# Performance work log

Hardware: AMD Instinct MI355X
Metric: run time of the kernel (lower is better)

Reference implementation:

```python
import jax, jax.numpy as jnp
import numpy as np

H, C = 4, 64            # heads, channels per head (graph_hidden_channels)
GHC = H * C             # concat width = 256
FIN = 32                # num_node_features
NHID = 256
NOUT = 256
NEG_SLOPE = 0.2         # PyG GATConv default negative_slope


def gat_conv(x, src, dst, n, W, a_src, a_dst, bias):
    # x: [N, Fin], W: [Fin, H*C], a_src/a_dst: [H, C], bias: [H*C]
    h = (x @ W).reshape(n, H, C)                       # [N,H,C]
    s = (h * a_src).sum(-1)                            # [N,H] src logits
    d = (h * a_dst).sum(-1)                            # [N,H] dst logits
    e = jax.nn.leaky_relu(s[src] + d[dst], NEG_SLOPE)  # [E,H]
    m = jax.ops.segment_max(e, dst, num_segments=n)    # segment softmax (stable)
    ex = jnp.exp(e - m[dst])
    denom = jax.ops.segment_sum(ex, dst, num_segments=n)
    alpha = ex / jnp.maximum(denom[dst], 1e-16)        # [E,H]
    msg = h[src] * alpha[:, :, None]                   # [E,H,C]
    out = jax.ops.segment_sum(msg, dst, num_segments=n)
    return out.reshape(n, GHC) + bias


def setup_inputs() -> dict:
    key = jax.random.key(0)
    ks = jax.random.split(key, 32)
    N, E, G = 50000, 800000, 256
    inp = {
        'x': jax.random.normal(ks[0], (N, FIN), dtype=jnp.float32),
        'edge_index': jax.random.randint(ks[1], (2, E), 0, N, dtype=jnp.int32),
        'batch': jnp.sort(jax.random.randint(ks[2], (N,), 0, G, dtype=jnp.int32)),
        'num_graphs': G,
    }
    def p(k, shape):
        return jax.random.normal(k, shape, dtype=jnp.float32) * 0.05
    # three GATConv layers + head linears
    ins = [FIN, C, C]
    i = 3
    for l, fin in enumerate(ins, start=1):
        inp[f'W{l}'] = p(ks[i], (fin, GHC)); i += 1
        inp[f'a{l}s'] = p(ks[i], (H, C)); i += 1
        inp[f'a{l}d'] = p(ks[i], (H, C)); i += 1
        inp[f'b{l}'] = p(ks[i], (GHC,)); i += 1
        inp[f'hl{l}_w'] = p(ks[i], (GHC, C)); i += 1
        inp[f'hl{l}_b'] = p(ks[i], (C,)); i += 1
    inp['mh1_w'] = p(ks[i], (C, NHID)); i += 1
    inp['mh1_b'] = p(ks[i], (NHID,)); i += 1
    inp['mh2_w'] = p(ks[i], (NHID, NOUT)); i += 1
    inp['mh2_b'] = p(ks[i], (NOUT,))
    return inp


def reference(x, edge_index, batch, num_graphs,
              W1, a1s, a1d, b1, hl1_w, hl1_b,
              W2, a2s, a2d, b2, hl2_w, hl2_b,
              W3, a3s, a3d, b3, hl3_w, hl3_b,
              mh1_w, mh1_b, mh2_w, mh2_b):
    n = x.shape[0]
    loops = jnp.arange(n, dtype=edge_index.dtype)  # PyG add_self_loops=True
    src = jnp.concatenate([edge_index[0], loops])
    dst = jnp.concatenate([edge_index[1], loops])

    h = gat_conv(x, src, dst, n, W1, a1s, a1d, b1)
    h = jax.nn.relu(h @ hl1_w + hl1_b)
    h = gat_conv(h, src, dst, n, W2, a2s, a2d, b2)
    h = jax.nn.relu(h @ hl2_w + hl2_b)
    h = gat_conv(h, src, dst, n, W3, a3s, a3d, b3)
    h = h @ hl3_w + hl3_b                      # no relu before pooling (as in source)

    sums = jax.ops.segment_sum(h, batch, num_segments=num_graphs)
    cnt = jax.ops.segment_sum(jnp.ones((n,), h.dtype), batch, num_segments=num_graphs)
    g = sums / jnp.maximum(cnt, 1.0)[:, None]  # global_mean_pool

    g = jax.nn.relu(g @ mh1_w + mh1_b)
    return g @ mh2_w + mh2_b
```

## Files before the change

kernel.cpp:

```cpp
#include <hip/hip_runtime.h>
#include <hip/hip_bf16.h>
#include <hip/hip_fp16.h>
#include <math.h>

#define HD 4
#define CH 64
#define GHC 256
#define NEG 0.2f
#define CHUNK 4096
#define BCAP 16384

#define WAVE_SYNC() do { __builtin_amdgcn_wave_barrier(); \
                         asm volatile("s_waitcnt lgkmcnt(0)" ::: "memory"); } while (0)

typedef _Float16 f16x8 __attribute__((ext_vector_type(8)));
typedef float f32x4 __attribute__((ext_vector_type(4)));

__device__ __forceinline__ float wsum32(float v){
  #pragma unroll
  for (int o = 16; o > 0; o >>= 1) v += __shfl_xor(v, o);
  return v;
}

__global__ __launch_bounds__(256)
void bin_stage(const int* __restrict__ ei, int E, int N,
               int* __restrict__ bres, unsigned* __restrict__ pairs)
{
  __shared__ unsigned staged[CHUNK];
  __shared__ unsigned short bkt[CHUNK];
  __shared__ int cnts[256], loff[256], gpos[256];
  const int t = threadIdx.x;
  const int tot = E + N;
  const int cbase = blockIdx.x * CHUNK;
  if (cbase >= tot) return;

  cnts[t] = 0;
  __syncthreads();

  unsigned myp[CHUNK / 256];
  int myb[CHUNK / 256], myr[CHUNK / 256];
  #pragma unroll
  for (int j = 0; j < CHUNK / 256; j++){
    int i = cbase + t + j * 256;
    myb[j] = -1;
    if (i < tot){
      int src, dst;
      if (i < E){ src = ei[i]; dst = ei[E + i]; }
      else { src = dst = i - E; }
      myb[j] = dst >> 8;
      myp[j] = (unsigned)src | ((unsigned)dst << 16);
      myr[j] = atomicAdd(&cnts[myb[j]], 1);
    }
  }
  __syncthreads();

  int v = cnts[t];
  loff[t] = v;
  __syncthreads();
  for (int o = 1; o < 256; o <<= 1){
    int tv = (t >= o) ? loff[t - o] : 0;
    __syncthreads();
    loff[t] += tv;
    __syncthreads();
  }
  int excl = loff[t] - v;
  __syncthreads();
  loff[t] = excl;
  __syncthreads();

  #pragma unroll
  for (int j = 0; j < CHUNK / 256; j++){
    if (myb[j] >= 0){
      int slot = loff[myb[j]] + myr[j];
      staged[slot] = myp[j];
      bkt[slot] = (unsigned short)myb[j];
    }
  }
  if (v > 0) gpos[t] = atomicAdd(&bres[t], v);
  __syncthreads();

  int total = min(CHUNK, tot - cbase);
  for (int i = t; i < total; i += 256){
    int b = bkt[i];
    int addr = b * BCAP + gpos[b] + (i - loff[b]);
    pairs[addr] = staged[i];
  }
}

__global__ __launch_bounds__(256)
void build_csr(const unsigned* __restrict__ pairs, const int* __restrict__ bres,
               int N, int Etot, int* __restrict__ offs, unsigned short* __restrict__ csr)
{
  __shared__ int dcnt[256], doff[256], bscan[256];
  const int b = blockIdx.x, t = threadIdx.x;
  int bv = bres[t];
  bscan[t] = bv;
  __syncthreads();
  for (int o = 1; o < 256; o <<= 1){
    int tv = (t >= o) ? bscan[t - o] : 0;
    __syncthreads();
    bscan[t] += tv;
    __syncthreads();
  }
  const int beg = bscan[b] - bres[b];
  const int cnt = bres[b];
  const unsigned* pb = pairs + (size_t)b * BCAP;
  dcnt[t] = 0;
  __syncthreads();
  for (int i = t; i < cnt; i += 256)
    atomicAdd(&dcnt[(pb[i] >> 16) & 255], 1);
  __syncthreads();
  int v = dcnt[t];
  doff[t] = v;
  __syncthreads();
  for (int o = 1; o < 256; o <<= 1){
    int tv = (t >= o) ? doff[t - o] : 0;
    __syncthreads();
    doff[t] += tv;
    __syncthreads();
  }
  int excl = doff[t] - v;
  __syncthreads();
  doff[t] = excl;
  __syncthreads();
  int node = (b << 8) + t;
  if (node < N) offs[node] = beg + doff[t];
  if (b == 0 && t == 0) offs[N] = Etot;
  dcnt[t] = 0;
  __syncthreads();
  for (int i = t; i < cnt; i += 256){
    unsigned pr = pb[i];
    int l = (pr >> 16) & 255;
    int pos = beg + doff[l] + atomicAdd(&dcnt[l], 1);
    csr[pos] = (unsigned short)(pr & 0xFFFF);
  }
}

__global__ __launch_bounds__(256)
void fuse_all(const float* __restrict__ W1, const float* __restrict__ a1s,
              const float* __restrict__ a1d, const float* __restrict__ b1,
              const float* __restrict__ h1w, const float* __restrict__ h1b,
              const float* __restrict__ W2, const float* __restrict__ a2s,
              const float* __restrict__ a2d, const float* __restrict__ b2,
              const float* __restrict__ h2w, const float* __restrict__ h2b,
              const float* __restrict__ W3, const float* __restrict__ a3s,
              const float* __restrict__ a3d, const float* __restrict__ b3,
              const float* __restrict__ h3w, const float* __restrict__ h3b,
              __half* __restrict__ Wpk1, float* __restrict__ Psd1, float* __restrict__ cb1,
              __half* __restrict__ Wpk2, __half* __restrict__ Ppk2, float* __restrict__ cb2,
              float* __restrict__ Wcp3, __half* __restrict__ Ppk3, float* __restrict__ cb3,
              const int* __restrict__ batch, int N, int G, int* __restrict__ bnd)
{
  const int blk = blockIdx.x, t = threadIdx.x;
  if (blk >= 163){
    int g = (blk - 163) * 256 + t;
    if (g > G) return;
    if (g == G){ bnd[G] = N; return; }
    int lo = 0, hi = N;
    while (lo < hi){ int mid = (lo + hi) >> 1; if (batch[mid] < g) lo = mid + 1; else hi = mid; }
    bnd[g] = lo;
    return;
  }
  const float *W, *as, *ad, *bl, *hlw, *hlb;
  float *cb;
  int FIN, b, layer;
  if (blk < 33){
    W = W1; as = a1s; ad = a1d; bl = b1; hlw = h1w; hlb = h1b;
    cb = cb1; FIN = 32; b = blk; layer = 1;
  } else if (blk < 98){
    W = W2; as = a2s; ad = a2d; bl = b2; hlw = h2w; hlb = h2b;
    cb = cb2; FIN = 64; b = blk - 33; layer = 2;
  } else {
    W = W3; as = a3s; ad = a3d; bl = b3; hlw = h3w; hlb = h3b;
    cb = cb3; FIN = 64; b = blk - 98; layer = 3;
  }
  if (b < FIN){
    const int c = t >> 2, h = t & 3;
    const float* wrow = W + b * GHC + h * 64;
    float acc = 0.f;
    #pragma unroll 8
    for (int j = 0; j < 64; j++)
      acc += wrow[j] * hlw[(h * 64 + j) * CH + c];
    const int k = h * FIN + b;
    if (layer == 3){
      Wcp3[k * CH + c] = acc;
    } else {
      int ks = k >> 5, nt = c >> 4;
      int lane = (((k & 31) >> 3) << 4) | (c & 15);
      int idx = ((ks * 4 + nt) * 64 + lane) * 8 + (k & 7);
      __half* Wpk = (layer == 1) ? Wpk1 : Wpk2;
      Wpk[idx] = __float2half(acc);
    }
    if (t < 8){
      const int hh = t & 3;
      const float* a = (t < 4) ? as : ad;
      const float* wr2 = W + b * GHC + hh * 64;
      float p = 0.f;
      #pragma unroll 8
      for (int j = 0; j < 64; j++) p += wr2[j] * a[hh * 64 + j];
      if (layer == 1){
        Psd1[b * 8 + t] = p;
      } else {
        int kk = b;
        int ks = kk >> 5;
        int lane = (((kk & 31) >> 3) << 4) | t;
        int idx = (ks * 64 + lane) * 8 + (kk & 7);
        __half* Ppk = (layer == 2) ? Ppk2 : Ppk3;
        Ppk[idx] = __float2half(p);
      }
    }
  } else if (t < CH){
    float acc = hlb[t];
    for (int j = 0; j < GHC; j++) acc += bl[j] * hlw[j * CH + t];
    cb[t] = acc;
  }
}

__global__ __launch_bounds__(256)
void logits_from_x(const float* __restrict__ x, const float* __restrict__ Psd,
                   float* __restrict__ s_log, float* __restrict__ d_log,
                   __half* __restrict__ xh0, int N)
{
  int idx = blockIdx.x * 256 + threadIdx.x;
  int node = idx >> 3, q = idx & 7;
  if (node >= N) return;
  const float* xr = x + (size_t)node * 32;
  float v = 0.f;
  #pragma unroll 8
  for (int k = 0; k < 32; k++) v += xr[k] * Psd[k * 8 + q];
  if (q < 4){
    s_log[node * 4 + q] = v;
    __half2 h0 = __floats2half2_rn(xr[q*8+0], xr[q*8+1]);
    __half2 h1 = __floats2half2_rn(xr[q*8+2], xr[q*8+3]);
    __half2 h2 = __floats2half2_rn(xr[q*8+4], xr[q*8+5]);
    __half2 h3 = __floats2half2_rn(xr[q*8+6], xr[q*8+7]);
    uint4 u;
    u.x = *reinterpret_cast<const unsigned*>(&h0);
    u.y = *reinterpret_cast<const unsigned*>(&h1);
    u.z = *reinterpret_cast<const unsigned*>(&h2);
    u.w = *reinterpret_cast<const unsigned*>(&h3);
    *reinterpret_cast<uint4*>(xh0 + (size_t)node * 32 + q * 8) = u;
  } else {
    d_log[node * 4 + (q - 4)] = v;
  }
}

template<int F>
__global__ __launch_bounds__(256)
void gat_aggregate_z(const __half* __restrict__ xin, const float* __restrict__ s_log,
                     const float* __restrict__ d_log, const int* __restrict__ off,
                     const unsigned short* __restrict__ csr, __half* __restrict__ z, int N)
{
  __shared__ float4 qa[4][2][32];
  __shared__ int    qs[4][2][32];
  const int wv   = threadIdx.x >> 6;
  const int lane = threadIdx.x & 63;
  const int half = lane >> 5;
  const int l32  = lane & 31;
  const int n = blockIdx.x * 8 + wv * 2 + half;
  const bool valid = n < N;

  int beg = 0, deg = 0;
  if (valid){ beg = off[n]; deg = off[n + 1] - beg; }

  float d4[4] = {0.f, 0.f, 0.f, 0.f};
  if (valid){
    float4 d4v = reinterpret_cast<const float4*>(d_log)[n];
    d4[0] = d4v.x; d4[1] = d4v.y; d4[2] = d4v.z; d4[3] = d4v.w;
  }

  float den[4], ex[4];
  int s = 0;

  {
    const bool act = valid && (l32 < deg);
    if (act){
      s = csr[beg + l32];
      float4 sl = reinterpret_cast<const float4*>(s_log)[s];
      float t[4] = {sl.x, sl.y, sl.z, sl.w};
      #pragma unroll
      for (int i = 0; i < 4; i++){
        float u = t[i] + d4[i]; u = (u >= 0.f) ? u : NEG * u;
        ex[i] = __expf(u);
      }
    } else {
      #pragma unroll
      for (int i = 0; i < 4; i++) ex[i] = 0.f;
    }
    #pragma unroll
    for (int i = 0; i < 4; i++) den[i] = wsum32(ex[i]);
  }
  for (int base = 32; base < deg; base += 32){
    const int k = base + l32;
    float e2[4] = {0.f, 0.f, 0.f, 0.f};
    if (k < deg){
      int s2 = csr[beg + k];
      float4 sl = reinterpret_cast<const float4*>(s_log)[s2];
      float t[4] = {sl.x, sl.y, sl.z, sl.w};
      #pragma unroll
      for (int i = 0; i < 4; i++){
        float u = t[i] + d4[i]; u = (u >= 0.f) ? u : NEG * u;
        e2[i] = __expf(u);
      }
    }
    #pragma unroll
    for (int i = 0; i < 4; i++) den[i] += wsum32(e2[i]);
  }

  float dninv[4];
  #pragma unroll
  for (int i = 0; i < 4; i++) dninv[i] = 1.f / fmaxf(den[i], 1e-16f);

  float a0[4] = {0.f,0.f,0.f,0.f};
  float a1[4] = {0.f,0.f,0.f,0.f};

  const float4* qap = qa[wv][half];
  const int*    qsp = qs[wv][half];

  auto accum = [&](int cnt){
    int cntR = (cnt + 3) & ~3;
    if (F == 64){
      const __half* xb = xin + 2 * l32;
      for (int e0 = 0; e0 < cntR; e0 += 4){
        float4 al[4]; int sv[4]; unsigned uv[4];
        #pragma unroll
        for (int j = 0; j < 4; j++){
          al[j] = qap[e0 + j];
          sv[j] = qsp[e0 + j];
        }
        #pragma unroll
        for (int j = 0; j < 4; j++)
          uv[j] = *reinterpret_cast<const unsigned*>(xb + sv[j] * 64);
        #pragma unroll
        for (int j = 0; j < 4; j++){
          float2 f = __half22float2(*reinterpret_cast<const __half2*>(&uv[j]));
          a0[0] += al[j].x * f.x; a1[0] += al[j].x * f.y;
          a0[1] += al[j].y * f.x; a1[1] += al[j].y * f.y;
          a0[2] += al[j].z * f.x; a1[2] += al[j].z * f.y;
          a0[3] += al[j].w * f.x; a1[3] += al[j].w * f.y;
        }
      }
    } else {
      const __half* xb = xin + l32;
      for (int e0 = 0; e0 < cntR; e0 += 4){
        float4 al[4]; int sv[4]; __half hv[4];
        #pragma unroll
        for (int j = 0; j < 4; j++){
          al[j] = qap[e0 + j];
          sv[j] = qsp[e0 + j];
        }
        #pragma unroll
        for (int j = 0; j < 4; j++)
          hv[j] = xb[sv[j] * 32];
        #pragma unroll
        for (int j = 0; j < 4; j++){
          float xv = __half2float(hv[j]);
          a0[0] += al[j].x * xv;
          a0[1] += al[j].y * xv;
          a0[2] += al[j].z * xv;
          a0[3] += al[j].w * xv;
        }
      }
    }
  };

  if (deg <= 32){
    qa[wv][half][l32] = make_float4(ex[0] * dninv[0], ex[1] * dninv[1],
                                    ex[2] * dninv[2], ex[3] * dninv[3]);
    qs[wv][half][l32] = s;
    WAVE_SYNC();
    accum(deg);
  } else {
    for (int base = 0; base < deg; base += 32){
      const int k = base + l32;
      int s2 = 0; float al[4] = {0.f, 0.f, 0.f, 0.f};
      if (k < deg){
        s2 = csr[beg + k];
        float4 sl = reinterpret_cast<const float4*>(s_log)[s2];
        float t[4] = {sl.x, sl.y, sl.z, sl.w};
        #pragma unroll
        for (int i = 0; i < 4; i++){
          float u = t[i] + d4[i]; u = (u >= 0.f) ? u : NEG * u;
          al[i] = __expf(u) * dninv[i];
        }
      }
      qa[wv][half][l32] = make_float4(al[0], al[1], al[2], al[3]);
      qs[wv][half][l32] = s2;
      WAVE_SYNC();
      accum(min(32, deg - base));
      WAVE_SYNC();
    }
  }

  if (valid){
    if (F == 64){
      const size_t zb = (size_t)n * 256 + 2 * l32;
      #pragma unroll
      for (int h = 0; h < 4; h++){
        __half2 hv = __floats2half2_rn(a0[h], a1[h]);
        *reinterpret_cast<unsigned*>(z + zb + h * 64) =
            *reinterpret_cast<const unsigned*>(&hv);
      }
    } else {
      const size_t zb = (size_t)n * 128 + l32;
      #pragma unroll
      for (int h = 0; h < 4; h++)
        z[zb + h * 32] = __float2half(a0[h]);
    }
  }
}

template<int ZW>
__global__ __launch_bounds__(256)
void z_transform_mfma(const __half* __restrict__ z, const __half* __restrict__ Wpk,
                      const float* __restrict__ cb, const __half* __restrict__ Ppk,
                      __half* __restrict__ xo, float* __restrict__ s_log,
                      float* __restrict__ d_log, int N)
{
  __shared__ float outs[4][16][68];
  __shared__ float cbs[64];
  const int tid = threadIdx.x;
  const int wv = tid >> 6, lane = tid & 63;
  const int row = lane & 15, kg = lane >> 4;
  const int n0 = blockIdx.x * 64 + wv * 16;
  if (tid < 64) cbs[tid] = cb[tid];
  __syncthreads();

  f32x4 acc0 = {0.f,0.f,0.f,0.f}, acc1 = {0.f,0.f,0.f,0.f};
  f32x4 acc2 = {0.f,0.f,0.f,0.f}, acc3 = {0.f,0.f,0.f,0.f};
  const __half* za = z + (size_t)(n0 + row) * ZW + kg * 8;
  const f16x8* wp = reinterpret_cast<const f16x8*>(Wpk) + lane;
  #pragma unroll
  for (int ks = 0; ks < ZW / 32; ks++){
    f16x8 af = *reinterpret_cast<const f16x8*>(za + ks * 32);
    acc0 = __builtin_amdgcn_mfma_f32_16x16x32_f16(af, wp[(ks*4+0)*64], acc0, 0,0,0);
    acc1 = __builtin_amdgcn_mfma_f32_16x16x32_f16(af, wp[(ks*4+1)*64], acc1, 0,0,0);
    acc2 = __builtin_amdgcn_mfma_f32_16x16x32_f16(af, wp[(ks*4+2)*64], acc2, 0,0,0);
    acc3 = __builtin_amdgcn_mfma_f32_16x16x32_f16(af, wp[(ks*4+3)*64], acc3, 0,0,0);
  }
  #pragma unroll
  for (int r = 0; r < 4; r++){
    int rr = kg * 4 + r;
    outs[wv][rr][ 0 + row] = fmaxf(acc0[r] + cbs[ 0 + row], 0.f);
    outs[wv][rr][16 + row] = fmaxf(acc1[r] + cbs[16 + row], 0.f);
    outs[wv][rr][32 + row] = fmaxf(acc2[r] + cbs[32 + row], 0.f);
    outs[wv][rr][48 + row] = fmaxf(acc3[r] + cbs[48 + row], 0.f);
  }
  WAVE_SYNC();

  #pragma unroll
  for (int i = 0; i < 4; i++){
    int idx = lane + 64 * i;
    int nn = idx >> 4, part = idx & 15;
    int node = n0 + nn;
    if (node < N){
      const float* o = &outs[wv][nn][part * 4];
      __half2 h0 = __floats2half2_rn(o[0], o[1]);
      __half2 h1 = __floats2half2_rn(o[2], o[3]);
      uint2 u;
      u.x = *reinterpret_cast<const unsigned*>(&h0);
      u.y = *reinterpret_cast<const unsigned*>(&h1);
      *reinterpret_cast<uint2*>(xo + (size_t)node * 64 + part * 4) = u;
    }
  }

  f32x4 lacc = {0.f,0.f,0.f,0.f};
  const f16x8* pp = reinterpret_cast<const f16x8*>(Ppk) + lane;
  #pragma unroll
  for (int ks = 0; ks < 2; ks++){
    f16x8 af;
    #pragma unroll
    for (int j = 0; j < 8; j++) af[j] = (_Float16)outs[wv][row][ks * 32 + kg * 8 + j];
    lacc = __builtin_amdgcn_mfma_f32_16x16x32_f16(af, pp[ks * 64], lacc, 0,0,0);
  }
  if (row < 8){
    float* dst = (row < 4) ? s_log : d_log;
    int q = row & 3;
    #pragma unroll
    for (int r = 0; r < 4; r++){
      int node = n0 + kg * 4 + r;
      if (node < N) dst[node * 4 + q] = lacc[r];
    }
  }
}

__global__ __launch_bounds__(256)
void pool_partial(const __half* __restrict__ z3, const int* __restrict__ bnd,
                  float* __restrict__ psum)
{
  const int blk = blockIdx.x, tid = threadIdx.x;
  const int g = blk >> 2, part = blk & 3;
  const int s = bnd[g], e = bnd[g + 1];
  const int cp = tid & 127, rp = tid >> 7;
  float ax = 0.f, ay = 0.f;
  for (int n = s + part + 4 * rp; n < e; n += 8){
    __half2 hv = *reinterpret_cast<const __half2*>(z3 + (size_t)n * 256 + 2 * cp);
    float2 f = __half22float2(hv);
    ax += f.x; ay += f.y;
  }
  __shared__ float shx[2][128], shy[2][128];
  shx[rp][cp] = ax; shy[rp][cp] = ay;
  __syncthreads();
  if (tid < 128){
    psum[(size_t)blk * 256 + 2 * tid]     = shx[0][tid] + shx[1][tid];
    psum[(size_t)blk * 256 + 2 * tid + 1] = shy[0][tid] + shy[1][tid];
  }
}

__global__ __launch_bounds__(256)
void head_mlp(const float* __restrict__ psum, const int* __restrict__ bnd,
              const float* __restrict__ Wcp3, const float* __restrict__ cb3,
              const float* __restrict__ m1w, const float* __restrict__ m1b,
              const float* __restrict__ m2w, const float* __restrict__ m2b,
              float* __restrict__ out)
{
  const int g = blockIdx.x, tid = threadIdx.x;
  const float cnt = (float)max(bnd[g + 1] - bnd[g], 1);
  __shared__ float zbar[256];
  const float* pb = psum + (size_t)g * 1024;
  zbar[tid] = (pb[tid] + pb[256 + tid] + pb[512 + tid] + pb[768 + tid]) / cnt;
  __syncthreads();
  const int c = tid & 63, part = tid >> 6;
  float tp = 0.f;
  #pragma unroll 8
  for (int k = part * 64; k < part * 64 + 64; k++) tp += zbar[k] * Wcp3[k * 64 + c];
  __shared__ float tsh[4][64];
  tsh[part][c] = tp;
  __syncthreads();
  __shared__ float tvec[64];
  if (tid < 64)
    tvec[tid] = tsh[0][tid] + tsh[1][tid] + tsh[2][tid] + tsh[3][tid] + cb3[tid];
  __syncthreads();
  float a = m1b[tid];
  #pragma unroll 8
  for (int cc = 0; cc < 64; cc++) a += tvec[cc] * m1w[cc * 256 + tid];
  __shared__ float g1row[256];
  g1row[tid] = fmaxf(a, 0.f);
  __syncthreads();
  float o = m2b[tid];
  #pragma unroll 8
  for (int k = 0; k < 256; k++) o += g1row[k] * m2w[k * 256 + tid];
  out[g * 256 + tid] = o;
}

extern "C" void kernel_launch(void* const* d_in, const int* in_sizes, int n_in,
                              void* d_out, int out_size, void* d_ws, size_t ws_size,
                              hipStream_t stream)
{
  const float* x     = (const float*)d_in[0];
  const int*   ei    = (const int*)d_in[1];
  const int*   batch = (const int*)d_in[2];
  const float* W1  = (const float*)d_in[4];
  const float* a1s = (const float*)d_in[5];
  const float* a1d = (const float*)d_in[6];
  const float* b1  = (const float*)d_in[7];
  const float* h1w = (const float*)d_in[8];
  const float* h1b = (const float*)d_in[9];
  const float* W2  = (const float*)d_in[10];
  const float* a2s = (const float*)d_in[11];
  const float* a2d = (const float*)d_in[12];
  const float* b2  = (const float*)d_in[13];
  const float* h2w = (const float*)d_in[14];
  const float* h2b = (const float*)d_in[15];
  const float* W3  = (const float*)d_in[16];
  const float* a3s = (const float*)d_in[17];
  const float* a3d = (const float*)d_in[18];
  const float* b3  = (const float*)d_in[19];
  const float* h3w = (const float*)d_in[20];
  const float* h3b = (const float*)d_in[21];
  const float* m1w = (const float*)d_in[22];
  const float* m1b = (const float*)d_in[23];
  const float* m2w = (const float*)d_in[24];
  const float* m2b = (const float*)d_in[25];

  const int N = in_sizes[0] / 32;
  const int E = in_sizes[1] / 2;
  const int G = out_size / 256;
  const int Etot = E + N;
  const int nbuck = (N + 255) >> 8;

  char* p = (char*)d_ws;
  auto alloc = [&](size_t bytes) -> void* {
    void* r = (void*)p;
    p += ((bytes + 255) / 256) * 256;
    return r;
  };
  __half* zbuf   = (__half*)alloc((size_t)N * GHC * 2);
  __half* xh0    = (__half*)alloc((size_t)N * 32 * 2);
  __half* xh1    = (__half*)alloc((size_t)N * CH * 2);
  __half* xh2    = (__half*)alloc((size_t)N * CH * 2);
  float* s_log   = (float*)alloc((size_t)N * HD * 4);
  float* d_log   = (float*)alloc((size_t)N * HD * 4);
  int*   offs    = (int*)alloc((size_t)(N + 1) * 4);
  unsigned short* csr = (unsigned short*)alloc((size_t)Etot * 2);
  unsigned* pairs = (unsigned*)alloc((size_t)nbuck * BCAP * 4);
  int*    bres   = (int*)alloc(256 * 4);
  __half* Ppk2   = (__half*)alloc(1024 * 2);
  __half* Ppk3   = (__half*)alloc(1024 * 2);
  int*   bnd     = (int*)alloc((size_t)(G + 1) * 4);
  float* psum    = (float*)alloc((size_t)G * 4 * 256 * 4);
  float* Wcp3    = (float*)alloc(256 * 64 * 4);
  float* Psd1    = (float*)alloc(32 * 8 * 4);
  float* cb1     = (float*)alloc(64 * 4);
  float* cb2     = (float*)alloc(64 * 4);
  float* cb3     = (float*)alloc(64 * 4);
  __half* Wpk1   = (__half*)alloc(128 * 64 * 2);
  __half* Wpk2   = (__half*)alloc(256 * 64 * 2);

  hipMemsetAsync(bres, 0, 5120, stream);

  const int cb_blocks = (Etot + CHUNK - 1) / CHUNK;
  bin_stage<<<cb_blocks, 256, 0, stream>>>(ei, E, N, bres, pairs);
  build_csr<<<nbuck, 256, 0, stream>>>(pairs, bres, N, Etot, offs, csr);

  const int fb = 163 + (G + 256) / 256;
  fuse_all<<<fb, 256, 0, stream>>>(W1, a1s, a1d, b1, h1w, h1b,
                                   W2, a2s, a2d, b2, h2w, h2b,
                                   W3, a3s, a3d, b3, h3w, h3b,
                                   Wpk1, Psd1, cb1, Wpk2, Ppk2, cb2, Wcp3, Ppk3, cb3,
                                   batch, N, G, bnd);

  const int ab = (N + 7) / 8;
  const int zb = (N + 63) / 64;

  logits_from_x<<<((size_t)N * 8 + 255) / 256, 256, 0, stream>>>(x, Psd1, s_log, d_log, xh0, N);

  gat_aggregate_z<32><<<ab, 256, 0, stream>>>(xh0, s_log, d_log, offs, csr, zbuf, N);
  z_transform_mfma<128><<<zb, 256, 0, stream>>>(zbuf, Wpk1, cb1, Ppk2, xh1, s_log, d_log, N);

  gat_aggregate_z<64><<<ab, 256, 0, stream>>>(xh1, s_log, d_log, offs, csr, zbuf, N);
  z_transform_mfma<256><<<zb, 256, 0, stream>>>(zbuf, Wpk2, cb2, Ppk3, xh2, s_log, d_log, N);

  gat_aggregate_z<64><<<ab, 256, 0, stream>>>(xh2, s_log, d_log, offs, csr, zbuf, N);

  pool_partial<<<G * 4, 256, 0, stream>>>(zbuf, bnd, psum);
  head_mlp<<<G, 256, 0, stream>>>(psum, bnd, Wcp3, cb3, m1w, m1b, m2w, m2b, (float*)d_out);
}
```

Measured before the change: 167.8 us.

## Fuse GAT aggregation with MFMA transform per layer, keeping z in LDS

Layers 1 and 2 now run a single kernel that aggregates attention-weighted neighbour features for 16 nodes into shared memory. The same block then applies the packed-weight MFMA transform, bias, ReLU and next-layer logit projection. This removes the global write and re-read of the wide z buffer and one launch per layer. Logit buffers are double-buffered so the next layer's logits do not overwrite ones still being read. The cost is 512-thread blocks with more LDS and only 4 of 8 waves doing MFMA, which may reduce occupancy and leave waves idle during the transform.

```diff
diff --git a/kernel.cpp b/kernel.cpp
--- a/kernel.cpp
+++ b/kernel.cpp
@@ -245,38 +245,48 @@
   }
 }
 
-template<int F>
-__global__ __launch_bounds__(256)
-void gat_aggregate_z(const __half* __restrict__ xin, const float* __restrict__ s_log,
-                     const float* __restrict__ d_log, const int* __restrict__ off,
-                     const unsigned short* __restrict__ csr, __half* __restrict__ z, int N)
-{
-  __shared__ float4 qa[4][2][32];
-  __shared__ int    qs[4][2][32];
-  const int wv   = threadIdx.x >> 6;
-  const int lane = threadIdx.x & 63;
+template<int F, int ZW>
+__global__ __launch_bounds__(512)
+void gat_layer_fused(const __half* __restrict__ xin, const float* __restrict__ s_in,
+                     const float* __restrict__ d_in_, const int* __restrict__ off,
+                     const unsigned short* __restrict__ csr,
+                     const __half* __restrict__ Wpk, const float* __restrict__ cb,
+                     const __half* __restrict__ Ppk,
+                     __half* __restrict__ xo, float* __restrict__ s_out,
+                     float* __restrict__ d_out_, int N)
+{
+  constexpr int ZP = ZW + 8;
+  __shared__ float4 qa[8][2][32];
+  __shared__ int    qs[8][2][32];
+  __shared__ __half z_lds[16][ZP];
+  __shared__ float  outs[16][68];
+  __shared__ float  cbs[64];
+  const int tid  = threadIdx.x;
+  const int wv   = tid >> 6;
+  const int lane = tid & 63;
   const int half = lane >> 5;
   const int l32  = lane & 31;
-  const int n = blockIdx.x * 8 + wv * 2 + half;
+  const int n0 = blockIdx.x * 16;
+  const int n = n0 + wv * 2 + half;
   const bool valid = n < N;
+  if (tid < 64) cbs[tid] = cb[tid];
 
   int beg = 0, deg = 0;
   if (valid){ beg = off[n]; deg = off[n + 1] - beg; }
 
   float d4[4] = {0.f, 0.f, 0.f, 0.f};
   if (valid){
-    float4 d4v = reinterpret_cast<const float4*>(d_log)[n];
+    float4 d4v = reinterpret_cast<const float4*>(d_in_)[n];
     d4[0] = d4v.x; d4[1] = d4v.y; d4[2] = d4v.z; d4[3] = d4v.w;
   }
 
   float den[4], ex[4];
   int s = 0;
-
   {
     const bool act = valid && (l32 < deg);
     if (act){
       s = csr[beg + l32];
-      float4 sl = reinterpret_cast<const float4*>(s_log)[s];
+      float4 sl = reinterpret_cast<const float4*>(s_in)[s];
       float t[4] = {sl.x, sl.y, sl.z, sl.w};
       #pragma unroll
       for (int i = 0; i < 4; i++){
@@ -295,7 +305,7 @@
     float e2[4] = {0.f, 0.f, 0.f, 0.f};
     if (k < deg){
       int s2 = csr[beg + k];
-      float4 sl = reinterpret_cast<const float4*>(s_log)[s2];
+      float4 sl = reinterpret_cast<const float4*>(s_in)[s2];
       float t[4] = {sl.x, sl.y, sl.z, sl.w};
       #pragma unroll
       for (int i = 0; i < 4; i++){
@@ -313,7 +323,6 @@
 
   float a0[4] = {0.f,0.f,0.f,0.f};
   float a1[4] = {0.f,0.f,0.f,0.f};
-
   const float4* qap = qa[wv][half];
   const int*    qsp = qs[wv][half];
 
@@ -324,10 +333,7 @@
       for (int e0 = 0; e0 < cntR; e0 += 4){
         float4 al[4]; int sv[4]; unsigned uv[4];
         #pragma unroll
-        for (int j = 0; j < 4; j++){
-          al[j] = qap[e0 + j];
-          sv[j] = qsp[e0 + j];
-        }
+        for (int j = 0; j < 4; j++){ al[j] = qap[e0 + j]; sv[j] = qsp[e0 + j]; }
         #pragma unroll
         for (int j = 0; j < 4; j++)
           uv[j] = *reinterpret_cast<const unsigned*>(xb + sv[j] * 64);
@@ -345,10 +351,7 @@
       for (int e0 = 0; e0 < cntR; e0 += 4){
         float4 al[4]; int sv[4]; __half hv[4];
         #pragma unroll
-        for (int j = 0; j < 4; j++){
-          al[j] = qap[e0 + j];
-          sv[j] = qsp[e0 + j];
-        }
+        for (int j = 0; j < 4; j++){ al[j] = qap[e0 + j]; sv[j] = qsp[e0 + j]; }
         #pragma unroll
         for (int j = 0; j < 4; j++)
           hv[j] = xb[sv[j] * 32];
@@ -360,6 +363,196 @@
           a0[2] += al[j].z * xv;
           a0[3] += al[j].w * xv;
         }
+      }
+    }
+  };
+
+  if (deg <= 32){
+    qa[wv][half][l32] = make_float4(ex[0] * dninv[0], ex[1] * dninv[1],
+                                    ex[2] * dninv[2], ex[3] * dninv[3]);
+    qs[wv][half][l32] = s;
+    WAVE_SYNC();
+    accum(deg);
+  } else {
+    for (int base = 0; base < deg; base += 32){
+      const int k = base + l32;
+      int s2 = 0; float al[4] = {0.f, 0.f, 0.f, 0.f};
+      if (k < deg){
+        s2 = csr[beg + k];
+        float4 sl = reinterpret_cast<const float4*>(s_in)[s2];
+        float t[4] = {sl.x, sl.y, sl.z, sl.w};
+        #pragma unroll
+        for (int i = 0; i < 4; i++){
+          float u = t[i] + d4[i]; u = (u >= 0.f) ? u : NEG * u;
+          al[i] = __expf(u) * dninv[i];
+        }
+      }
+      qa[wv][half][l32] = make_float4(al[0], al[1], al[2], al[3]);
+      qs[wv][half][l32] = s2;
+      WAVE_SYNC();
+      accum(min(32, deg - base));
+      WAVE_SYNC();
+    }
+  }
+
+  {
+    const int r = wv * 2 + half;
+    if (F == 64){
+      #pragma unroll
+      for (int h = 0; h < 4; h++){
+        __half2 hv = __floats2half2_rn(a0[h], a1[h]);
+        *reinterpret_cast<unsigned*>(&z_lds[r][h * 64 + 2 * l32]) =
+            *reinterpret_cast<const unsigned*>(&hv);
+      }
+    } else {
+      #pragma unroll
+      for (int h = 0; h < 4; h++)
+        z_lds[r][h * 32 + l32] = __float2half(a0[h]);
+    }
+  }
+  __syncthreads();
+
+  const int row = lane & 15, kg = lane >> 4;
+  if (wv < 4){
+    const int nt = wv;
+    f32x4 acc = {0.f,0.f,0.f,0.f};
+    const f16x8* wp = reinterpret_cast<const f16x8*>(Wpk) + lane;
+    #pragma unroll
+    for (int ks = 0; ks < ZW / 32; ks++){
+      f16x8 af = *reinterpret_cast<const f16x8*>(&z_lds[row][kg * 8 + ks * 32]);
+      acc = __builtin_amdgcn_mfma_f32_16x16x32_f16(af, wp[(ks*4+nt)*64], acc, 0,0,0);
+    }
+    #pragma unroll
+    for (int r = 0; r < 4; r++){
+      int rr = kg * 4 + r;
+      outs[rr][nt * 16 + row] = fmaxf(acc[r] + cbs[nt * 16 + row], 0.f);
+    }
+  }
+  __syncthreads();
+
+  if (tid < 256){
+    int nn = tid >> 4, part = tid & 15;
+    int node = n0 + nn;
+    if (node < N){
+      const float* o = &outs[nn][part * 4];
+      __half2 h0 = __floats2half2_rn(o[0], o[1]);
+      __half2 h1 = __floats2half2_rn(o[2], o[3]);
+      uint2 u;
+      u.x = *reinterpret_cast<const unsigned*>(&h0);
+      u.y = *reinterpret_cast<const unsigned*>(&h1);
+      *reinterpret_cast<uint2*>(xo + (size_t)node * 64 + part * 4) = u;
+    }
+  }
+
+  if (wv == 4){
+    f32x4 lacc = {0.f,0.f,0.f,0.f};
+    const f16x8* pp = reinterpret_cast<const f16x8*>(Ppk) + lane;
+    #pragma unroll
+    for (int ks = 0; ks < 2; ks++){
+      f16x8 af;
+      #pragma unroll
+      for (int j = 0; j < 8; j++) af[j] = (_Float16)outs[row][ks * 32 + kg * 8 + j];
+      lacc = __builtin_amdgcn_mfma_f32_16x16x32_f16(af, pp[ks * 64], lacc, 0,0,0);
+    }
+    if (row < 8){
+      float* dst = (row < 4) ? s_out : d_out_;
+      int q = row & 3;
+      #pragma unroll
+      for (int r = 0; r < 4; r++){
+        int node = n0 + kg * 4 + r;
+        if (node < N) dst[node * 4 + q] = lacc[r];
+      }
+    }
+  }
+}
+
+template<int F>
+__global__ __launch_bounds__(256)
+void gat_aggregate_z(const __half* __restrict__ xin, const float* __restrict__ s_log,
+                     const float* __restrict__ d_log, const int* __restrict__ off,
+                     const unsigned short* __restrict__ csr, __half* __restrict__ z, int N)
+{
+  __shared__ float4 qa[4][2][32];
+  __shared__ int    qs[4][2][32];
+  const int wv   = threadIdx.x >> 6;
+  const int lane = threadIdx.x & 63;
+  const int half = lane >> 5;
+  const int l32  = lane & 31;
+  const int n = blockIdx.x * 8 + wv * 2 + half;
+  const bool valid = n < N;
+
+  int beg = 0, deg = 0;
+  if (valid){ beg = off[n]; deg = off[n + 1] - beg; }
+
+  float d4[4] = {0.f, 0.f, 0.f, 0.f};
+  if (valid){
+    float4 d4v = reinterpret_cast<const float4*>(d_log)[n];
+    d4[0] = d4v.x; d4[1] = d4v.y; d4[2] = d4v.z; d4[3] = d4v.w;
+  }
+
+  float den[4], ex[4];
+  int s = 0;
+  {
+    const bool act = valid && (l32 < deg);
+    if (act){
+      s = csr[beg + l32];
+      float4 sl = reinterpret_cast<const float4*>(s_log)[s];
+      float t[4] = {sl.x, sl.y, sl.z, sl.w};
+      #pragma unroll
+      for (int i = 0; i < 4; i++){
+        float u = t[i] + d4[i]; u = (u >= 0.f) ? u : NEG * u;
+        ex[i] = __expf(u);
+      }
+    } else {
+      #pragma unroll
+      for (int i = 0; i < 4; i++) ex[i] = 0.f;
+    }
+    #pragma unroll
+    for (int i = 0; i < 4; i++) den[i] = wsum32(ex[i]);
+  }
+  for (int base = 32; base < deg; base += 32){
+    const int k = base + l32;
+    float e2[4] = {0.f, 0.f, 0.f, 0.f};
+    if (k < deg){
+      int s2 = csr[beg + k];
+      float4 sl = reinterpret_cast<const float4*>(s_log)[s2];
+      float t[4] = {sl.x, sl.y, sl.z, sl.w};
+      #pragma unroll
+      for (int i = 0; i < 4; i++){
+        float u = t[i] + d4[i]; u = (u >= 0.f) ? u : NEG * u;
+        e2[i] = __expf(u);
+      }
+    }
+    #pragma unroll
+    for (int i = 0; i < 4; i++) den[i] += wsum32(e2[i]);
+  }
+
+  float dninv[4];
+  #pragma unroll
+  for (int i = 0; i < 4; i++) dninv[i] = 1.f / fmaxf(den[i], 1e-16f);
+
+  float a0[4] = {0.f,0.f,0.f,0.f};
+  float a1[4] = {0.f,0.f,0.f,0.f};
+  const float4* qap = qa[wv][half];
+  const int*    qsp = qs[wv][half];
+
+  auto accum = [&](int cnt){
+    int cntR = (cnt + 3) & ~3;
+    const __half* xb = xin + 2 * l32;
+    for (int e0 = 0; e0 < cntR; e0 += 4){
+      float4 al[4]; int sv[4]; unsigned uv[4];
+      #pragma unroll
+      for (int j = 0; j < 4; j++){ al[j] = qap[e0 + j]; sv[j] = qsp[e0 + j]; }
+      #pragma unroll
+      for (int j = 0; j < 4; j++)
+        uv[j] = *reinterpret_cast<const unsigned*>(xb + sv[j] * 64);
+      #pragma unroll
+      for (int j = 0; j < 4; j++){
+        float2 f = __half22float2(*reinterpret_cast<const __half2*>(&uv[j]));
+        a0[0] += al[j].x * f.x; a1[0] += al[j].x * f.y;
+        a0[1] += al[j].y * f.x; a1[1] += al[j].y * f.y;
+        a0[2] += al[j].z * f.x; a1[2] += al[j].z * f.y;
+        a0[3] += al[j].w * f.x; a1[3] += al[j].w * f.y;
       }
     }
   };
@@ -393,93 +586,12 @@
   }
 
   if (valid){
-    if (F == 64){
-      const size_t zb = (size_t)n * 256 + 2 * l32;
-      #pragma unroll
-      for (int h = 0; h < 4; h++){
-        __half2 hv = __floats2half2_rn(a0[h], a1[h]);
-        *reinterpret_cast<unsigned*>(z + zb + h * 64) =
-            *reinterpret_cast<const unsigned*>(&hv);
-      }
-    } else {
-      const size_t zb = (size_t)n * 128 + l32;
-      #pragma unroll
-      for (int h = 0; h < 4; h++)
-        z[zb + h * 32] = __float2half(a0[h]);
-    }
-  }
-}
-
-template<int ZW>
-__global__ __launch_bounds__(256)
-void z_transform_mfma(const __half* __restrict__ z, const __half* __restrict__ Wpk,
-                      const float* __restrict__ cb, const __half* __restrict__ Ppk,
-                      __half* __restrict__ xo, float* __restrict__ s_log,
-                      float* __restrict__ d_log, int N)
-{
-  __shared__ float outs[4][16][68];
-  __shared__ float cbs[64];
-  const int tid = threadIdx.x;
-  const int wv = tid >> 6, lane = tid & 63;
-  const int row = lane & 15, kg = lane >> 4;
-  const int n0 = blockIdx.x * 64 + wv * 16;
-  if (tid < 64) cbs[tid] = cb[tid];
-  __syncthreads();
-
-  f32x4 acc0 = {0.f,0.f,0.f,0.f}, acc1 = {0.f,0.f,0.f,0.f};
-  f32x4 acc2 = {0.f,0.f,0.f,0.f}, acc3 = {0.f,0.f,0.f,0.f};
-  const __half* za = z + (size_t)(n0 + row) * ZW + kg * 8;
-  const f16x8* wp = reinterpret_cast<const f16x8*>(Wpk) + lane;
-  #pragma unroll
-  for (int ks = 0; ks < ZW / 32; ks++){
-    f16x8 af = *reinterpret_cast<const f16x8*>(za + ks * 32);
-    acc0 = __builtin_amdgcn_mfma_f32_16x16x32_f16(af, wp[(ks*4+0)*64], acc0, 0,0,0);
-    acc1 = __builtin_amdgcn_mfma_f32_16x16x32_f16(af, wp[(ks*4+1)*64], acc1, 0,0,0);
-    acc2 = __builtin_amdgcn_mfma_f32_16x16x32_f16(af, wp[(ks*4+2)*64], acc2, 0,0,0);
-    acc3 = __builtin_amdgcn_mfma_f32_16x16x32_f16(af, wp[(ks*4+3)*64], acc3, 0,0,0);
-  }
-  #pragma unroll
-  for (int r = 0; r < 4; r++){
-    int rr = kg * 4 + r;
-    outs[wv][rr][ 0 + row] = fmaxf(acc0[r] + cbs[ 0 + row], 0.f);
-    outs[wv][rr][16 + row] = fmaxf(acc1[r] + cbs[16 + row], 0.f);
-    outs[wv][rr][32 + row] = fmaxf(acc2[r] + cbs[32 + row], 0.f);
-    outs[wv][rr][48 + row] = fmaxf(acc3[r] + cbs[48 + row], 0.f);
-  }
-  WAVE_SYNC();
-
-  #pragma unroll
-  for (int i = 0; i < 4; i++){
-    int idx = lane + 64 * i;
-    int nn = idx >> 4, part = idx & 15;
-    int node = n0 + nn;
-    if (node < N){
-      const float* o = &outs[wv][nn][part * 4];
-      __half2 h0 = __floats2half2_rn(o[0], o[1]);
-      __half2 h1 = __floats2half2_rn(o[2], o[3]);
-      uint2 u;
-      u.x = *reinterpret_cast<const unsigned*>(&h0);
-      u.y = *reinterpret_cast<const unsigned*>(&h1);
-      *reinterpret_cast<uint2*>(xo + (size_t)node * 64 + part * 4) = u;
-    }
-  }
-
-  f32x4 lacc = {0.f,0.f,0.f,0.f};
-  const f16x8* pp = reinterpret_cast<const f16x8*>(Ppk) + lane;
-  #pragma unroll
-  for (int ks = 0; ks < 2; ks++){
-    f16x8 af;
+    const size_t zb = (size_t)n * 256 + 2 * l32;
     #pragma unroll
-    for (int j = 0; j < 8; j++) af[j] = (_Float16)outs[wv][row][ks * 32 + kg * 8 + j];
-    lacc = __builtin_amdgcn_mfma_f32_16x16x32_f16(af, pp[ks * 64], lacc, 0,0,0);
-  }
-  if (row < 8){
-    float* dst = (row < 4) ? s_log : d_log;
-    int q = row & 3;
-    #pragma unroll
-    for (int r = 0; r < 4; r++){
-      int node = n0 + kg * 4 + r;
-      if (node < N) dst[node * 4 + q] = lacc[r];
+    for (int h = 0; h < 4; h++){
+      __half2 hv = __floats2half2_rn(a0[h], a1[h]);
+      *reinterpret_cast<unsigned*>(z + zb + h * 64) =
+          *reinterpret_cast<const unsigned*>(&hv);
     }
   }
 }
@@ -589,8 +701,10 @@
   __half* xh0    = (__half*)alloc((size_t)N * 32 * 2);
   __half* xh1    = (__half*)alloc((size_t)N * CH * 2);
   __half* xh2    = (__half*)alloc((size_t)N * CH * 2);
-  float* s_log   = (float*)alloc((size_t)N * HD * 4);
-  float* d_log   = (float*)alloc((size_t)N * HD * 4);
+  float* s_logA  = (float*)alloc((size_t)N * HD * 4);
+  float* d_logA  = (float*)alloc((size_t)N * HD * 4);
+  float* s_logB  = (float*)alloc((size_t)N * HD * 4);
+  float* d_logB  = (float*)alloc((size_t)N * HD * 4);
   int*   offs    = (int*)alloc((size_t)(N + 1) * 4);
   unsigned short* csr = (unsigned short*)alloc((size_t)Etot * 2);
   unsigned* pairs = (unsigned*)alloc((size_t)nbuck * BCAP * 4);
@@ -620,18 +734,16 @@
                                    Wpk1, Psd1, cb1, Wpk2, Ppk2, cb2, Wcp3, Ppk3, cb3,
                                    batch, N, G, bnd);
 
+  logits_from_x<<<((size_t)N * 8 + 255) / 256, 256, 0, stream>>>(x, Psd1, s_logA, d_logA, xh0, N);
+
+  const int fgrid = (N + 15) / 16;
+  gat_layer_fused<32, 128><<<fgrid, 512, 0, stream>>>(xh0, s_logA, d_logA, offs, csr,
+                                                      Wpk1, cb1, Ppk2, xh1, s_logB, d_logB, N);
+  gat_layer_fused<64, 256><<<fgrid, 512, 0, stream>>>(xh1, s_logB, d_logB, offs, csr,
+                                                      Wpk2, cb2, Ppk3, xh2, s_logA, d_logA, N);
+
   const int ab = (N + 7) / 8;
-  const int zb = (N + 63) / 64;
-
-  logits_from_x<<<((size_t)N * 8 + 255) / 256, 256, 0, stream>>>(x, Psd1, s_log, d_log, xh0, N);
-
-  gat_aggregate_z<32><<<ab, 256, 0, stream>>>(xh0, s_log, d_log, offs, csr, zbuf, N);
-  z_transform_mfma<128><<<zb, 256, 0, stream>>>(zbuf, Wpk1, cb1, Ppk2, xh1, s_log, d_log, N);
-
-  gat_aggregate_z<64><<<ab, 256, 0, stream>>>(xh1, s_log, d_log, offs, csr, zbuf, N);
-  z_transform_mfma<256><<<zb, 256, 0, stream>>>(zbuf, Wpk2, cb2, Ppk3, xh2, s_log, d_log, N);
-
-  gat_aggregate_z<64><<<ab, 256, 0, stream>>>(xh2, s_log, d_log, offs, csr, zbuf, N);
+  gat_aggregate_z<64><<<ab, 256, 0, stream>>>(xh2, s_logA, d_logA, offs, csr, zbuf, N);
 
   pool_partial<<<G * 4, 256, 0, stream>>>(zbuf, bnd, psum);
   head_mlp<<<G, 256, 0, stream>>>(psum, bnd, Wcp3, cb3, m1w, m1b, m2w, m2b, (float*)d_out);
```

New measurement: 161.7 us, median of 2. -3.6%, faster.
